# Kernel tuning notes

Hardware: AMD Instinct MI355X
Metric: run time of the kernel (lower is better)

The kernel has to match this reference:

```python
import jax, jax.numpy as jnp
import numpy as np

B, N, D, H = 2, 512, 384, 12
SQK, SV, PQ, PV = 16, 16, 4, 8
SCALE = 1.0 / np.sqrt(SQK + 4 * PQ)  # attention_scale, point_pair_dim=4
EPS = 1e-12


def setup_inputs() -> dict:
    key = jax.random.key(0)
    ks = jax.random.split(key, 10)

    def w(k, fan_in, fan_out):
        return (jax.random.normal(k, (fan_in, fan_out), jnp.float32) / np.sqrt(fan_in))

    return {
        "hidden": jax.random.normal(ks[0], (B, N, D), jnp.float32),
        "xyz": jax.random.normal(ks[1], (B, N, 3), jnp.float32),
        "W_qk": w(ks[2], D, 2 * H * SQK), "b_qk": jnp.zeros((2 * H * SQK,), jnp.float32),
        "W_vs": w(ks[3], D, H * SV), "b_vs": jnp.zeros((H * SV,), jnp.float32),
        "W_so": w(ks[4], H * SV, D), "b_so": jnp.zeros((D,), jnp.float32),
        "W_pqk": w(ks[5], D, H * PQ * 3), "b_pqk": jnp.zeros((H * PQ * 3,), jnp.float32),
        "W_pv": w(ks[6], D, H * PV * 3), "b_pv": jnp.zeros((H * PV * 3,), jnp.float32),
        "W_po": w(ks[7], H * PV * 3, D), "b_po": jnp.zeros((D,), jnp.float32),
        "W_fp": w(ks[8], 2 * D, D), "b_fp": jnp.zeros((D,), jnp.float32),
    }


def reference(hidden, xyz, W_qk, b_qk, W_vs, b_vs, W_so, b_so,
              W_pqk, b_pqk, W_pv, b_pv, W_po, b_po, W_fp, b_fp):
    # scalar q/k/v (note: heads are NOT split in the attention matmuls, per source)
    qk = hidden @ W_qk + b_qk                       # [B,N,2*H*SQK]
    q_s, k_s = jnp.split(qk, 2, axis=-1)            # [B,N,H*SQK] each
    v_s = hidden @ W_vs + b_vs                      # [B,N,H*SV]

    # points; k_points = q_points in source
    qp = (hidden @ W_pqk + b_pqk).reshape(B, N, H, PQ, 3)
    vp = hidden @ W_pv + b_pv                       # [B,N,H*PV*3]

    scalar_attn = jnp.einsum('bid,bjd->bij', q_s, k_s)  # [B,N,N]

    # fused pairwise point features: dist(q_i, k_j) + sum of 3 cosine components
    # = dist + cos_sim, per (head, point); avoid materializing [B,N,N,H,P,3].
    dot = jnp.einsum('bihpc,bjhpc->bijhp', qp, qp)      # [B,N,N,H,PQ]
    n2 = jnp.sum(qp * qp, axis=-1)                      # [B,N,H,PQ]
    d2 = n2[:, :, None] + n2[:, None] - 2.0 * dot
    dist = jnp.sqrt(jnp.maximum(d2, 0.0) + EPS)
    nrm = jnp.sqrt(n2 + EPS)
    cos = dot / (nrm[:, :, None] * nrm[:, None])
    point_attn = jnp.sum(dist + cos, axis=(-1, -2))     # [B,N,N]

    attn = jax.nn.softmax((scalar_attn + point_attn) * SCALE, axis=-1)

    scalar_result = jnp.einsum('bij,bjd->bid', attn, v_s)   # [B,N,H*SV]
    point_result = jnp.einsum('bij,bjd->bid', attn, vp)     # [B,N,H*PV*3]

    scalar_result = scalar_result @ W_so + b_so             # [B,N,D]
    point_result = point_result @ W_po + b_po               # [B,N,D]

    result = jnp.concatenate([scalar_result, point_result], axis=-1) @ W_fp + b_fp
    delta_xyz = point_result.reshape(B, N, -1, 3).mean(axis=2)  # [B,N,3]
    return result, xyz + delta_xyz
```

## Files before the change

kernel.cpp:

```cpp
#include <hip/hip_runtime.h>
#include <math.h>

typedef unsigned short u16;
typedef __attribute__((ext_vector_type(8))) short bf16x8;
typedef __attribute__((ext_vector_type(4))) float f32x4;

#define BB 2
#define NN 512
#define SCALEF 0.17677669529663687f

__device__ __forceinline__ u16 f2bf(float x) {
  union { float f; unsigned u; } c; c.f = x;
  unsigned r = (c.u + 0x7FFFu + ((c.u >> 16) & 1u)) >> 16;
  return (u16)r;
}
__device__ __forceinline__ float bf2f(u16 h) {
  union { unsigned u; float f; } c; c.u = ((unsigned)h) << 16;
  return c.f;
}
__device__ __forceinline__ void pack8(const float* v, bf16x8& h, bf16x8& l) {
#pragma unroll
  for (int j = 0; j < 8; ++j) {
    u16 hi = f2bf(v[j]);
    h[j] = (short)hi;
    l[j] = (short)f2bf(v[j] - bf2f(hi));
  }
}
#define MFMA3(ACC, AH, AL, BH, BL)                                              \
  ACC = __builtin_amdgcn_mfma_f32_16x16x32_bf16(AH, BH, ACC, 0, 0, 0);          \
  ACC = __builtin_amdgcn_mfma_f32_16x16x32_bf16(AH, BL, ACC, 0, 0, 0);          \
  ACC = __builtin_amdgcn_mfma_f32_16x16x32_bf16(AL, BH, ACC, 0, 0, 0);

template<int MR, int NF>
__device__ __forceinline__ void mfma_tile(
    const u16* __restrict__ Ah, const u16* __restrict__ Al, int lda,
    const u16* __restrict__ Bh, const u16* __restrict__ Bl, int ldb,
    int kBeg, int kEnd, int arow, int bcol, f32x4 (&acc)[MR][NF]) {
  const int lane = threadIdx.x & 63;
  const int rr = lane & 15, kg = lane >> 4;
  const u16* pah = Ah + (size_t)(arow + rr) * lda + kg * 8;
  const u16* pal = Al + (size_t)(arow + rr) * lda + kg * 8;
  const u16* pbh = Bh + (size_t)(bcol + rr) * ldb + kg * 8;
  const u16* pbl = Bl + (size_t)(bcol + rr) * ldb + kg * 8;
#pragma unroll 2
  for (int k0 = kBeg; k0 < kEnd; k0 += 32) {
    bf16x8 a_h[MR], a_l[MR], b_h[NF], b_l[NF];
#pragma unroll
    for (int m = 0; m < MR; ++m) {
      a_h[m] = *(const bf16x8*)(pah + (size_t)m * 16 * lda + k0);
      a_l[m] = *(const bf16x8*)(pal + (size_t)m * 16 * lda + k0);
    }
#pragma unroll
    for (int f = 0; f < NF; ++f) {
      b_h[f] = *(const bf16x8*)(pbh + (size_t)f * 16 * ldb + k0);
      b_l[f] = *(const bf16x8*)(pbl + (size_t)f * 16 * ldb + k0);
    }
#pragma unroll
    for (int m = 0; m < MR; ++m)
#pragma unroll
      for (int f = 0; f < NF; ++f) { MFMA3(acc[m][f], a_h[m], a_l[m], b_h[f], b_l[f]) }
  }
}

__global__ __launch_bounds__(512) void k_input(
    const float* __restrict__ hidden, const float* __restrict__ xyz,
    const float* __restrict__ W_qk, const float* __restrict__ b_qk,
    const float* __restrict__ W_vs, const float* __restrict__ b_vs,
    const float* __restrict__ W_pv, const float* __restrict__ b_pv,
    const float* __restrict__ W_pqk, const float* __restrict__ b_pqk,
    u16* __restrict__ QKh, u16* __restrict__ QKl,
    u16* __restrict__ VTh, u16* __restrict__ VTl,
    float* __restrict__ QPf, float* __restrict__ out_xyz) {
  __shared__ f32x4 CB[7][2][3][64];
  __shared__ u16 Dh[48][32], Dl[48][32];
  const int tid = threadIdx.x;
  const int w = tid >> 6, lane = tid & 63;
  const int rr = lane & 15, kg = lane >> 4;
  const int row0 = blockIdx.y * 32, col0 = blockIdx.x * 48;

  if (blockIdx.x == 18) {
    for (int t2 = tid; t2 < 96; t2 += 512)
      out_xyz[(size_t)row0 * 3 + t2] = xyz[(size_t)row0 * 3 + t2];
  }

  const float* W; const float* bias; int Ns, region;
  if (col0 < 384)      { W = W_qk;  Ns = 384; bias = b_qk + col0;          W += col0;       region = 0; }
  else if (col0 < 576) { W = W_vs;  Ns = 192; bias = b_vs + (col0 - 384);  W += col0 - 384; region = 1; }
  else if (col0 < 864) { W = W_pv;  Ns = 288; bias = b_pv + (col0 - 576);  W += col0 - 576; region = 1; }
  else                 { W = W_pqk; Ns = 144; bias = b_pqk + (col0 - 864); W += col0 - 864; region = 2; }

  f32x4 acc[2][3] = {};
  const float* pa = hidden + (size_t)(row0 + rr) * 384 + kg * 8;
  const float* pw = W + rr;
  for (int k0 = w * 32; k0 < 384; k0 += 256) {
    bf16x8 a_h[2], a_l[2], b_h[3], b_l[3];
#pragma unroll
    for (int m = 0; m < 2; ++m) {
      float v[8];
      *(float4*)&v[0] = *(const float4*)(pa + (size_t)m * 16 * 384 + k0);
      *(float4*)&v[4] = *(const float4*)(pa + (size_t)m * 16 * 384 + k0 + 4);
      pack8(v, a_h[m], a_l[m]);
    }
    const float* bp0 = pw + (size_t)(k0 + kg * 8) * Ns;
#pragma unroll
    for (int f = 0; f < 3; ++f) {
      float v[8];
#pragma unroll
      for (int j = 0; j < 8; ++j) v[j] = bp0[(size_t)j * Ns + f * 16];
      pack8(v, b_h[f], b_l[f]);
    }
#pragma unroll
    for (int m = 0; m < 2; ++m)
#pragma unroll
      for (int f = 0; f < 3; ++f) { MFMA3(acc[m][f], a_h[m], a_l[m], b_h[f], b_l[f]) }
  }
  if (w) {
#pragma unroll
    for (int m = 0; m < 2; ++m)
#pragma unroll
      for (int f = 0; f < 3; ++f) CB[w - 1][m][f][lane] = acc[m][f];
  }
  __syncthreads();
  if (w) return;
#pragma unroll
  for (int wv = 0; wv < 7; ++wv)
#pragma unroll
    for (int m = 0; m < 2; ++m)
#pragma unroll
      for (int f = 0; f < 3; ++f) acc[m][f] += CB[wv][m][f][lane];

  const int rb = (lane >> 4) << 2, cc = lane & 15;
  if (region == 0) {
#pragma unroll
    for (int f = 0; f < 3; ++f) {
      int n = col0 + f * 16 + cc;
      float bv = bias[f * 16 + cc];
#pragma unroll
      for (int m = 0; m < 2; ++m)
#pragma unroll
        for (int r = 0; r < 4; ++r) {
          float v = acc[m][f][r] + bv;
          int row = row0 + m * 16 + rb + r;
          u16 hi = f2bf(v);
          QKh[(size_t)row * 384 + n] = hi;
          QKl[(size_t)row * 384 + n] = f2bf(v - bf2f(hi));
        }
    }
  } else if (region == 2) {
#pragma unroll
    for (int f = 0; f < 3; ++f) {
      int c = (col0 - 864) + f * 16 + cc;
      float bv = bias[f * 16 + cc];
#pragma unroll
      for (int m = 0; m < 2; ++m)
#pragma unroll
        for (int r = 0; r < 4; ++r)
          QPf[(size_t)(row0 + m * 16 + rb + r) * 144 + c] = acc[m][f][r] + bv;
    }
  } else {
#pragma unroll
    for (int f = 0; f < 3; ++f) {
      float bv = bias[f * 16 + cc];
#pragma unroll
      for (int m = 0; m < 2; ++m)
#pragma unroll
        for (int r = 0; r < 4; ++r) {
          float v = acc[m][f][r] + bv;
          u16 hi = f2bf(v);
          Dh[f * 16 + cc][m * 16 + rb + r] = hi;
          Dl[f * 16 + cc][m * 16 + rb + r] = f2bf(v - bf2f(hi));
        }
    }
    const int b = row0 >> 9, rl = row0 & 511;
    const int cbase = col0 - 384;
    u16* dsth = VTh + (size_t)b * 480 * 512;
    u16* dstl = VTl + (size_t)b * 480 * 512;
    for (int u = lane; u < 192; u += 64) {
      int c = u >> 2, seg = u & 3;
      *(uint4*)(dsth + (size_t)(cbase + c) * 512 + rl + seg * 8) = *(const uint4*)&Dh[c][seg * 8];
      *(uint4*)(dstl + (size_t)(cbase + c) * 512 + rl + seg * 8) = *(const uint4*)&Dl[c][seg * 8];
    }
  }
}

#define PROW 244
__global__ __launch_bounds__(512) void k_attn(
    const u16* __restrict__ QKh, const u16* __restrict__ QKl,
    const float* __restrict__ QPf, float* __restrict__ ATTf) {
  __shared__ float Pi[32][PROW];
  __shared__ float Pj[32][PROW];
  __shared__ float Sf[2][32 * 33];
  const int b = blockIdx.z;
  int t = blockIdx.x, ti_ = 0;
  while (t >= 16 - ti_) { t -= 16 - ti_; ++ti_; }
  const int tj_ = ti_ + t;
  const int i0 = ti_ * 32, j0 = tj_ * 32;
  const bool offdiag = (tj_ != ti_);
  const int tid = threadIdx.x;
  for (int u = tid; u < 3072; u += 512) {
    int side = (u >= 1536) ? 1 : 0;
    int rem = u - side * 1536;
    int row = rem / 48, hp = rem - row * 48;
    int grow = b * NN + (side ? j0 : i0) + row;
    const float* p = QPf + (size_t)grow * 144 + hp * 3;
    float x = p[0], y = p[1], z = p[2];
    float n2 = x * x + y * y + z * z;
    float inv = __frsqrt_rn(n2 + 1e-12f);
    float* dst = side ? &Pj[row][0] : &Pi[row][0];
    ((float4*)dst)[hp] = make_float4(x, y, z, n2);
    dst[192 + hp] = inv;
  }
  __syncthreads();
  const int h = tid >> 8;
  const int t8 = tid & 255;
  const int tj = t8 & 15, ti = t8 >> 4;
  {
    float a00 = 0.f, a01 = 0.f, a10 = 0.f, a11 = 0.f;
    const float4* A0 = (const float4*)&Pi[ti][0];
    const float4* A1 = (const float4*)&Pi[ti + 16][0];
    const float4* B0 = (const float4*)&Pj[tj][0];
    const float4* B1 = (const float4*)&Pj[tj + 16][0];
    const float* iA0 = &Pi[ti][192];
    const float* iA1 = &Pi[ti + 16][192];
    const float* iB0 = &Pj[tj][192];
    const float* iB1 = &Pj[tj + 16][192];
    const int hpB = h * 24, hpE = hpB + 24;
#pragma unroll 4
    for (int hp = hpB; hp < hpE; ++hp) {
      float4 p0 = A0[hp], p1 = A1[hp], q0 = B0[hp], q1 = B1[hp];
      float va0 = iA0[hp], va1 = iA1[hp], vb0 = iB0[hp], vb1 = iB1[hp];
      {
        float dot = p0.x * q0.x + p0.y * q0.y + p0.z * q0.z;
        float d2 = fmaxf(fmaf(-2.f, dot, p0.w + q0.w), 0.f) + 1e-12f;
        a00 += d2 * __frsqrt_rn(d2) + dot * (va0 * vb0);
      }
      {
        float dot = p0.x * q1.x + p0.y * q1.y + p0.z * q1.z;
        float d2 = fmaxf(fmaf(-2.f, dot, p0.w + q1.w), 0.f) + 1e-12f;
        a01 += d2 * __frsqrt_rn(d2) + dot * (va0 * vb1);
      }
      {
        float dot = p1.x * q0.x + p1.y * q0.y + p1.z * q0.z;
        float d2 = fmaxf(fmaf(-2.f, dot, p1.w + q0.w), 0.f) + 1e-12f;
        a10 += d2 * __frsqrt_rn(d2) + dot * (va1 * vb0);
      }
      {
        float dot = p1.x * q1.x + p1.y * q1.y + p1.z * q1.z;
        float d2 = fmaxf(fmaf(-2.f, dot, p1.w + q1.w), 0.f) + 1e-12f;
        a11 += d2 * __frsqrt_rn(d2) + dot * (va1 * vb1);
      }
    }
    Sf[h][ti * 33 + tj] = a00;
    Sf[h][ti * 33 + tj + 16] = a01;
    Sf[h][(ti + 16) * 33 + tj] = a10;
    Sf[h][(ti + 16) * 33 + tj + 16] = a11;
  }
  const int w = tid >> 6, lane = tid & 63;
  const int dir = w >> 2, sub = w & 3;
  f32x4 q[1][1] = {};
  if (dir == 0) {
    int arow = b * NN + i0 + (sub >> 1) * 16;
    int brow = b * NN + j0 + (sub & 1) * 16;
    mfma_tile<1, 1>(QKh, QKl, 384, QKh + 192, QKl + 192, 384, 0, 192, arow, brow, q);
  } else if (offdiag) {
    int arow = b * NN + j0 + (sub >> 1) * 16;
    int brow = b * NN + i0 + (sub & 1) * 16;
    mfma_tile<1, 1>(QKh, QKl, 384, QKh + 192, QKl + 192, 384, 0, 192, arow, brow, q);
  }
  __syncthreads();
  const int rl = (sub >> 1) * 16 + ((lane >> 4) << 2);
  const int cl = (sub & 1) * 16 + (lane & 15);
  float* Cb = ATTf + (size_t)b * NN * NN;
  if (dir == 0) {
#pragma unroll
    for (int r = 0; r < 4; ++r)
      Cb[(size_t)(i0 + rl + r) * NN + j0 + cl] =
          q[0][0][r] + Sf[0][(rl + r) * 33 + cl] + Sf[1][(rl + r) * 33 + cl];
  } else if (offdiag) {
#pragma unroll
    for (int r = 0; r < 4; ++r)
      Cb[(size_t)(j0 + rl + r) * NN + i0 + cl] =
          q[0][0][r] + Sf[0][cl * 33 + rl + r] + Sf[1][cl * 33 + rl + r];
  }
}

__global__ __launch_bounds__(512) void k_pv(
    const float* __restrict__ ATTf,
    const u16* __restrict__ VTh, const u16* __restrict__ VTl,
    u16* __restrict__ SRh, u16* __restrict__ SRl) {
  __shared__ f32x4 CB[7][3][64];
  __shared__ float RS[7][64];
  const int tid = threadIdx.x;
  const int w = tid >> 6, lane = tid & 63;
  const int rr = lane & 15, kg = lane >> 4;
  const int b = blockIdx.z;
  const int row0 = blockIdx.y * 16, col0 = blockIdx.x * 48;
  const float* pa = ATTf + (size_t)(b * NN + row0 + rr) * NN + kg * 8;
  const u16* pbh = VTh + (size_t)b * 480 * 512 + (size_t)(col0 + rr) * 512 + kg * 8;
  const u16* pbl = VTl + (size_t)b * 480 * 512 + (size_t)(col0 + rr) * 512 + kg * 8;
  f32x4 acc[3] = {};
  float rs = 0.f;
  for (int k0 = w * 32; k0 < NN; k0 += 256) {
    bf16x8 a_h, a_l, b_h[3], b_l[3];
    {
      float v[8];
      *(float4*)&v[0] = *(const float4*)(pa + k0);
      *(float4*)&v[4] = *(const float4*)(pa + k0 + 4);
#pragma unroll
      for (int j = 0; j < 8; ++j) { float e = __expf(v[j] * SCALEF); rs += e; v[j] = e; }
      pack8(v, a_h, a_l);
    }
#pragma unroll
    for (int f = 0; f < 3; ++f) {
      b_h[f] = *(const bf16x8*)(pbh + (size_t)f * 16 * 512 + k0);
      b_l[f] = *(const bf16x8*)(pbl + (size_t)f * 16 * 512 + k0);
    }
#pragma unroll
    for (int f = 0; f < 3; ++f) { MFMA3(acc[f], a_h, a_l, b_h[f], b_l[f]) }
  }
  if (w) {
#pragma unroll
    for (int f = 0; f < 3; ++f) CB[w - 1][f][lane] = acc[f];
    RS[w - 1][lane] = rs;
  }
  __syncthreads();
  if (w) return;
#pragma unroll
  for (int wv = 0; wv < 7; ++wv) {
#pragma unroll
    for (int f = 0; f < 3; ++f) acc[f] += CB[wv][f][lane];
    rs += RS[wv][lane];
  }
  rs += __shfl_xor(rs, 16);
  rs += __shfl_xor(rs, 32);
  const int rb = (lane >> 4) << 2, cc = lane & 15;
  float inv[4];
#pragma unroll
  for (int r = 0; r < 4; ++r) inv[r] = 1.0f / __shfl(rs, rb + r);
  u16* oh = SRh + (size_t)b * NN * 480;
  u16* ol = SRl + (size_t)b * NN * 480;
#pragma unroll
  for (int f = 0; f < 3; ++f) {
    int n = col0 + f * 16 + cc;
#pragma unroll
    for (int r = 0; r < 4; ++r) {
      float v = acc[f][r] * inv[r];
      u16 hi = f2bf(v);
      oh[(size_t)(row0 + rb + r) * 480 + n] = hi;
      ol[(size_t)(row0 + rb + r) * 480 + n] = f2bf(v - bf2f(hi));
    }
  }
}

__global__ __launch_bounds__(512) void k_outproj(
    const u16* __restrict__ SRh, const u16* __restrict__ SRl,
    const float* __restrict__ W_so, const float* __restrict__ b_so,
    const float* __restrict__ W_po, const float* __restrict__ b_po,
    u16* __restrict__ PRh, u16* __restrict__ PRl, float* __restrict__ out_xyz) {
  __shared__ f32x4 CB[7][3][64];
  __shared__ float D[16][49];
  const int tid = threadIdx.x;
  const int w = tid >> 6, lane = tid & 63;
  const int rr = lane & 15, kg = lane >> 4;
  const int t = blockIdx.x;
  const int row0 = blockIdx.y * 16, col0 = t * 48;
  const float* W = (t < 8) ? W_so : W_po;
  const int kBeg = (t < 8) ? 0 : 192, kEnd = (t < 8) ? 192 : 480;
  const int wcol = (t < 8) ? col0 : col0 - 384;
  const u16* pah = SRh + (size_t)(row0 + rr) * 480 + kg * 8;
  const u16* pal = SRl + (size_t)(row0 + rr) * 480 + kg * 8;
  const float* pw = W + wcol + rr;
  f32x4 acc[3] = {};
  for (int k0 = kBeg + w * 32; k0 < kEnd; k0 += 256) {
    bf16x8 a_h, a_l, b_h[3], b_l[3];
    a_h = *(const bf16x8*)(pah + k0);
    a_l = *(const bf16x8*)(pal + k0);
    const float* bp0 = pw + (size_t)(k0 - kBeg + kg * 8) * 384;
#pragma unroll
    for (int f = 0; f < 3; ++f) {
      float v[8];
#pragma unroll
      for (int j = 0; j < 8; ++j) v[j] = bp0[(size_t)j * 384 + f * 16];
      pack8(v, b_h[f], b_l[f]);
    }
#pragma unroll
    for (int f = 0; f < 3; ++f) { MFMA3(acc[f], a_h, a_l, b_h[f], b_l[f]) }
  }
  if (w) {
#pragma unroll
    for (int f = 0; f < 3; ++f) CB[w - 1][f][lane] = acc[f];
  }
  __syncthreads();
  if (w) return;
#pragma unroll
  for (int wv = 0; wv < 7; ++wv)
#pragma unroll
    for (int f = 0; f < 3; ++f) acc[f] += CB[wv][f][lane];
  const int rb = (lane >> 4) << 2, cc = lane & 15;
#pragma unroll
  for (int f = 0; f < 3; ++f) {
    int n = col0 + f * 16 + cc;
    float bias = (n < 384) ? b_so[n] : b_po[n - 384];
#pragma unroll
    for (int r = 0; r < 4; ++r) {
      float v = acc[f][r] + bias;
      u16 hi = f2bf(v);
      PRh[(size_t)(row0 + rb + r) * 768 + n] = hi;
      PRl[(size_t)(row0 + rb + r) * 768 + n] = f2bf(v - bf2f(hi));
      if (t >= 8) D[rb + r][f * 16 + cc] = v;
    }
  }
  if (t >= 8 && lane < 16) {
    float sx = 0.f, sy = 0.f, sz = 0.f;
#pragma unroll
    for (int p = 0; p < 16; ++p) {
      sx += D[lane][3 * p];
      sy += D[lane][3 * p + 1];
      sz += D[lane][3 * p + 2];
    }
    int token = row0 + lane;
    atomicAdd(out_xyz + (size_t)token * 3 + 0, sx * (1.0f / 128.f));
    atomicAdd(out_xyz + (size_t)token * 3 + 1, sy * (1.0f / 128.f));
    atomicAdd(out_xyz + (size_t)token * 3 + 2, sz * (1.0f / 128.f));
  }
}

__global__ __launch_bounds__(512) void k_final(
    const u16* __restrict__ PRh, const u16* __restrict__ PRl,
    const float* __restrict__ W_fp, const float* __restrict__ b_fp,
    float* __restrict__ out_res) {
  __shared__ f32x4 CB[7][3][64];
  const int tid = threadIdx.x;
  const int w = tid >> 6, lane = tid & 63;
  const int rr = lane & 15, kg = lane >> 4;
  const int row0 = blockIdx.y * 16, col0 = blockIdx.x * 48;
  const u16* pah = PRh + (size_t)(row0 + rr) * 768 + kg * 8;
  const u16* pal = PRl + (size_t)(row0 + rr) * 768 + kg * 8;
  const float* pw = W_fp + col0 + rr;
  f32x4 acc[3] = {};
  for (int k0 = w * 32; k0 < 768; k0 += 256) {
    bf16x8 a_h, a_l, b_h[3], b_l[3];
    a_h = *(const bf16x8*)(pah + k0);
    a_l = *(const bf16x8*)(pal + k0);
    const float* bp0 = pw + (size_t)(k0 + kg * 8) * 384;
#pragma unroll
    for (int f = 0; f < 3; ++f) {
      float v[8];
#pragma unroll
      for (int j = 0; j < 8; ++j) v[j] = bp0[(size_t)j * 384 + f * 16];
      pack8(v, b_h[f], b_l[f]);
    }
#pragma unroll
    for (int f = 0; f < 3; ++f) { MFMA3(acc[f], a_h, a_l, b_h[f], b_l[f]) }
  }
  if (w) {
#pragma unroll
    for (int f = 0; f < 3; ++f) CB[w - 1][f][lane] = acc[f];
  }
  __syncthreads();
  if (w) return;
#pragma unroll
  for (int wv = 0; wv < 7; ++wv)
#pragma unroll
    for (int f = 0; f < 3; ++f) acc[f] += CB[wv][f][lane];
  const int rb = (lane >> 4) << 2, cc = lane & 15;
#pragma unroll
  for (int f = 0; f < 3; ++f) {
    int n = col0 + f * 16 + cc;
#pragma unroll
    for (int r = 0; r < 4; ++r)
      out_res[(size_t)(row0 + rb + r) * 384 + n] = acc[f][r] + b_fp[n];
  }
}

extern "C" void kernel_launch(void* const* d_in, const int* in_sizes, int n_in,
                              void* d_out, int out_size, void* d_ws, size_t ws_size,
                              hipStream_t stream) {
  const float* hidden = (const float*)d_in[0];
  const float* xyz   = (const float*)d_in[1];
  const float* W_qk  = (const float*)d_in[2];
  const float* b_qk  = (const float*)d_in[3];
  const float* W_vs  = (const float*)d_in[4];
  const float* b_vs  = (const float*)d_in[5];
  const float* W_so  = (const float*)d_in[6];
  const float* b_so  = (const float*)d_in[7];
  const float* W_pqk = (const float*)d_in[8];
  const float* b_pqk = (const float*)d_in[9];
  const float* W_pv  = (const float*)d_in[10];
  const float* b_pv  = (const float*)d_in[11];
  const float* W_po  = (const float*)d_in[12];
  const float* b_po  = (const float*)d_in[13];
  const float* W_fp  = (const float*)d_in[14];
  const float* b_fp  = (const float*)d_in[15];

  float* out_res = (float*)d_out;
  float* out_xyz = out_res + (size_t)BB * NN * 384;

  u16* p   = (u16*)d_ws;
  u16* QKh = p;            p += 393216;
  u16* QKl = p;            p += 393216;
  u16* VTh = p;            p += 491520;
  u16* VTl = p;            p += 491520;
  u16* SRh = p;            p += 491520;
  u16* SRl = p;            p += 491520;
  u16* PRh = p;            p += 786432;
  u16* PRl = p;            p += 786432;
  float* QPf  = (float*)p; p += 2 * 147456;
  float* ATTf = (float*)p;

  k_input<<<dim3(21, 32), 512, 0, stream>>>(hidden, xyz,
                                            W_qk, b_qk, W_vs, b_vs, W_pv, b_pv, W_pqk, b_pqk,
                                            QKh, QKl, VTh, VTl, QPf, out_xyz);
  k_attn<<<dim3(136, 1, 2), 512, 0, stream>>>(QKh, QKl, QPf, ATTf);
  k_pv<<<dim3(10, 32, 2), 512, 0, stream>>>(ATTf, VTh, VTl, SRh, SRl);
  k_outproj<<<dim3(16, 64), 512, 0, stream>>>(SRh, SRl, W_so, b_so, W_po, b_po,
                                              PRh, PRl, out_xyz);
  k_final<<<dim3(8, 64), 512, 0, stream>>>(PRh, PRl, W_fp, b_fp, out_res);
}
```

Before: 71.03 us.

## Fold output projections into final projection via precomputed combined weight matrix

The scalar and point output projections are composed with the final projection into a single 480x384 weight matrix, plus a combined bias and a reduced xyz-delta weight. Extra blocks in the input-projection kernel compute these each call. This removes one GEMM launch and the intermediate PR round trip through memory, so the tail becomes one GEMM with a small side path for xyz. The cost is extra weight-product work inside the first kernel, a bias loop that runs serially over 768 terms, and a change in rounding because the fused weights are split into bf16 hi/lo.

```diff
diff --git a/kernel.cpp b/kernel.cpp
--- a/kernel.cpp
+++ b/kernel.cpp
@@ -63,25 +63,99 @@
 }
 
 __global__ __launch_bounds__(512) void k_input(
-    const float* __restrict__ hidden, const float* __restrict__ xyz,
+    const float* __restrict__ hidden,
     const float* __restrict__ W_qk, const float* __restrict__ b_qk,
     const float* __restrict__ W_vs, const float* __restrict__ b_vs,
     const float* __restrict__ W_pv, const float* __restrict__ b_pv,
     const float* __restrict__ W_pqk, const float* __restrict__ b_pqk,
+    const float* __restrict__ W_so, const float* __restrict__ b_so,
+    const float* __restrict__ W_po, const float* __restrict__ b_po,
+    const float* __restrict__ W_fp, const float* __restrict__ b_fp,
     u16* __restrict__ QKh, u16* __restrict__ QKl,
     u16* __restrict__ VTh, u16* __restrict__ VTl,
-    float* __restrict__ QPf, float* __restrict__ out_xyz) {
+    float* __restrict__ QPf,
+    u16* __restrict__ WCTh, u16* __restrict__ WCTl,
+    float* __restrict__ bc, float* __restrict__ Wdf) {
+  const int tid = threadIdx.x;
+  if (blockIdx.x >= 21) {
+    const int cx = blockIdx.x - 21, ky = blockIdx.y;
+    if (cx < 8 && ky < 10) {
+      const int w = tid >> 6, lane = tid & 63;
+      if (w >= 3) return;
+      const int rr = lane & 15, kg = lane >> 4;
+      const int c0 = cx * 48;
+      const int kbase = ky * 48 + w * 16;
+      const float* Wop; int moff;
+      if (kbase < 192) { Wop = W_so + (size_t)kbase * 384; moff = 0; }
+      else             { Wop = W_po + (size_t)(kbase - 192) * 384; moff = 384; }
+      f32x4 acc[3] = {};
+      const float* pa = Wop + (size_t)rr * 384 + kg * 8;
+      const float* pw = W_fp + (size_t)moff * 384 + c0 + rr;
+      for (int m0 = 0; m0 < 384; m0 += 32) {
+        bf16x8 a_h, a_l, b_h[3], b_l[3];
+        float v[8];
+        *(float4*)&v[0] = *(const float4*)(pa + m0);
+        *(float4*)&v[4] = *(const float4*)(pa + m0 + 4);
+        pack8(v, a_h, a_l);
+        const float* bp0 = pw + (size_t)(m0 + kg * 8) * 384;
+#pragma unroll
+        for (int f = 0; f < 3; ++f) {
+          float u[8];
+#pragma unroll
+          for (int j = 0; j < 8; ++j) u[j] = bp0[(size_t)j * 384 + f * 16];
+          pack8(u, b_h[f], b_l[f]);
+        }
+#pragma unroll
+        for (int f = 0; f < 3; ++f) { MFMA3(acc[f], a_h, a_l, b_h[f], b_l[f]) }
+      }
+      const int rb = (lane >> 4) << 2, cc = lane & 15;
+#pragma unroll
+      for (int f = 0; f < 3; ++f) {
+        int c = c0 + f * 16 + cc;
+#pragma unroll
+        for (int r = 0; r < 4; ++r) {
+          int k = kbase + rb + r;
+          float vv = acc[f][r];
+          u16 hi = f2bf(vv);
+          WCTh[(size_t)c * 480 + k] = hi;
+          WCTl[(size_t)c * 480 + k] = f2bf(vv - bf2f(hi));
+        }
+      }
+      return;
+    }
+    if (cx == 0 && ky == 10) {
+      if (tid < 384) {
+        float s = b_fp[tid];
+        for (int m = 0; m < 384; ++m) s += b_so[m] * W_fp[(size_t)m * 384 + tid];
+        for (int m = 0; m < 384; ++m) s += b_po[m] * W_fp[(size_t)(384 + m) * 384 + tid];
+        bc[tid] = s;
+      }
+      return;
+    }
+    if (cx == 1 && ky == 10) {
+      for (int idx = tid; idx < 867; idx += 512) {
+        if (idx < 864) {
+          int j = idx / 3, c = idx - j * 3;
+          float s = 0.f;
+          for (int k = 0; k < 128; ++k) s += W_po[(size_t)j * 384 + 3 * k + c];
+          Wdf[idx] = s * (1.0f / 128.f);
+        } else {
+          int c = idx - 864;
+          float s = 0.f;
+          for (int k = 0; k < 128; ++k) s += b_po[3 * k + c];
+          Wdf[idx] = s * (1.0f / 128.f);
+        }
+      }
+      return;
+    }
+    return;
+  }
+
   __shared__ f32x4 CB[7][2][3][64];
   __shared__ u16 Dh[48][32], Dl[48][32];
-  const int tid = threadIdx.x;
   const int w = tid >> 6, lane = tid & 63;
   const int rr = lane & 15, kg = lane >> 4;
   const int row0 = blockIdx.y * 32, col0 = blockIdx.x * 48;
-
-  if (blockIdx.x == 18) {
-    for (int t2 = tid; t2 < 96; t2 += 512)
-      out_xyz[(size_t)row0 * 3 + t2] = xyz[(size_t)row0 * 3 + t2];
-  }
 
   const float* W; const float* bias; int Ns, region;
   if (col0 < 384)      { W = W_qk;  Ns = 384; bias = b_qk + col0;          W += col0;       region = 0; }
@@ -352,36 +426,51 @@
   }
 }
 
-__global__ __launch_bounds__(512) void k_outproj(
+__global__ __launch_bounds__(512) void k_tail(
     const u16* __restrict__ SRh, const u16* __restrict__ SRl,
-    const float* __restrict__ W_so, const float* __restrict__ b_so,
-    const float* __restrict__ W_po, const float* __restrict__ b_po,
-    u16* __restrict__ PRh, u16* __restrict__ PRl, float* __restrict__ out_xyz) {
+    const u16* __restrict__ WCTh, const u16* __restrict__ WCTl,
+    const float* __restrict__ bc, const float* __restrict__ Wdf,
+    const float* __restrict__ xyz,
+    float* __restrict__ out_res, float* __restrict__ out_xyz) {
+  const int tid = threadIdx.x;
+  const int row0 = blockIdx.y * 16;
+  if (blockIdx.x == 8) {
+    if (tid < 384) {
+      int out = tid >> 3, part = tid & 7;
+      int lt = out / 3, c = out - lt * 3;
+      int token = row0 + lt;
+      const u16* sh = SRh + (size_t)token * 480 + 192 + part * 36;
+      const u16* sl = SRl + (size_t)token * 480 + 192 + part * 36;
+      float s = 0.f;
+#pragma unroll 4
+      for (int kk = 0; kk < 36; ++kk) {
+        float v = bf2f(sh[kk]) + bf2f(sl[kk]);
+        s += v * Wdf[(part * 36 + kk) * 3 + c];
+      }
+#pragma unroll
+      for (int d = 4; d; d >>= 1) s += __shfl_down(s, d, 8);
+      if (part == 0)
+        out_xyz[(size_t)token * 3 + c] = xyz[(size_t)token * 3 + c] + s + Wdf[864 + c];
+    }
+    return;
+  }
   __shared__ f32x4 CB[7][3][64];
-  __shared__ float D[16][49];
-  const int tid = threadIdx.x;
   const int w = tid >> 6, lane = tid & 63;
   const int rr = lane & 15, kg = lane >> 4;
-  const int t = blockIdx.x;
-  const int row0 = blockIdx.y * 16, col0 = t * 48;
-  const float* W = (t < 8) ? W_so : W_po;
-  const int kBeg = (t < 8) ? 0 : 192, kEnd = (t < 8) ? 192 : 480;
-  const int wcol = (t < 8) ? col0 : col0 - 384;
+  const int col0 = blockIdx.x * 48;
   const u16* pah = SRh + (size_t)(row0 + rr) * 480 + kg * 8;
   const u16* pal = SRl + (size_t)(row0 + rr) * 480 + kg * 8;
-  const float* pw = W + wcol + rr;
+  const u16* pbh = WCTh + (size_t)(col0 + rr) * 480 + kg * 8;
+  const u16* pbl = WCTl + (size_t)(col0 + rr) * 480 + kg * 8;
   f32x4 acc[3] = {};
-  for (int k0 = kBeg + w * 32; k0 < kEnd; k0 += 256) {
+  for (int k0 = w * 32; k0 < 480; k0 += 256) {
     bf16x8 a_h, a_l, b_h[3], b_l[3];
     a_h = *(const bf16x8*)(pah + k0);
     a_l = *(const bf16x8*)(pal + k0);
-    const float* bp0 = pw + (size_t)(k0 - kBeg + kg * 8) * 384;
 #pragma unroll
     for (int f = 0; f < 3; ++f) {
-      float v[8];
-#pragma unroll
-      for (int j = 0; j < 8; ++j) v[j] = bp0[(size_t)j * 384 + f * 16];
-      pack8(v, b_h[f], b_l[f]);
+      b_h[f] = *(const bf16x8*)(pbh + (size_t)f * 16 * 480 + k0);
+      b_l[f] = *(const bf16x8*)(pbl + (size_t)f * 16 * 480 + k0);
     }
 #pragma unroll
     for (int f = 0; f < 3; ++f) { MFMA3(acc[f], a_h, a_l, b_h[f], b_l[f]) }
@@ -400,76 +489,9 @@
 #pragma unroll
   for (int f = 0; f < 3; ++f) {
     int n = col0 + f * 16 + cc;
-    float bias = (n < 384) ? b_so[n] : b_po[n - 384];
-#pragma unroll
-    for (int r = 0; r < 4; ++r) {
-      float v = acc[f][r] + bias;
-      u16 hi = f2bf(v);
-      PRh[(size_t)(row0 + rb + r) * 768 + n] = hi;
-      PRl[(size_t)(row0 + rb + r) * 768 + n] = f2bf(v - bf2f(hi));
-      if (t >= 8) D[rb + r][f * 16 + cc] = v;
-    }
-  }
-  if (t >= 8 && lane < 16) {
-    float sx = 0.f, sy = 0.f, sz = 0.f;
-#pragma unroll
-    for (int p = 0; p < 16; ++p) {
-      sx += D[lane][3 * p];
-      sy += D[lane][3 * p + 1];
-      sz += D[lane][3 * p + 2];
-    }
-    int token = row0 + lane;
-    atomicAdd(out_xyz + (size_t)token * 3 + 0, sx * (1.0f / 128.f));
-    atomicAdd(out_xyz + (size_t)token * 3 + 1, sy * (1.0f / 128.f));
-    atomicAdd(out_xyz + (size_t)token * 3 + 2, sz * (1.0f / 128.f));
-  }
-}
-
-__global__ __launch_bounds__(512) void k_final(
-    const u16* __restrict__ PRh, const u16* __restrict__ PRl,
-    const float* __restrict__ W_fp, const float* __restrict__ b_fp,
-    float* __restrict__ out_res) {
-  __shared__ f32x4 CB[7][3][64];
-  const int tid = threadIdx.x;
-  const int w = tid >> 6, lane = tid & 63;
-  const int rr = lane & 15, kg = lane >> 4;
-  const int row0 = blockIdx.y * 16, col0 = blockIdx.x * 48;
-  const u16* pah = PRh + (size_t)(row0 + rr) * 768 + kg * 8;
-  const u16* pal = PRl + (size_t)(row0 + rr) * 768 + kg * 8;
-  const float* pw = W_fp + col0 + rr;
-  f32x4 acc[3] = {};
-  for (int k0 = w * 32; k0 < 768; k0 += 256) {
-    bf16x8 a_h, a_l, b_h[3], b_l[3];
-    a_h = *(const bf16x8*)(pah + k0);
-    a_l = *(const bf16x8*)(pal + k0);
-    const float* bp0 = pw + (size_t)(k0 + kg * 8) * 384;
-#pragma unroll
-    for (int f = 0; f < 3; ++f) {
-      float v[8];
-#pragma unroll
-      for (int j = 0; j < 8; ++j) v[j] = bp0[(size_t)j * 384 + f * 16];
-      pack8(v, b_h[f], b_l[f]);
-    }
-#pragma unroll
-    for (int f = 0; f < 3; ++f) { MFMA3(acc[f], a_h, a_l, b_h[f], b_l[f]) }
-  }
-  if (w) {
-#pragma unroll
-    for (int f = 0; f < 3; ++f) CB[w - 1][f][lane] = acc[f];
-  }
-  __syncthreads();
-  if (w) return;
-#pragma unroll
-  for (int wv = 0; wv < 7; ++wv)
-#pragma unroll
-    for (int f = 0; f < 3; ++f) acc[f] += CB[wv][f][lane];
-  const int rb = (lane >> 4) << 2, cc = lane & 15;
-#pragma unroll
-  for (int f = 0; f < 3; ++f) {
-    int n = col0 + f * 16 + cc;
 #pragma unroll
     for (int r = 0; r < 4; ++r)
-      out_res[(size_t)(row0 + rb + r) * 384 + n] = acc[f][r] + b_fp[n];
+      out_res[(size_t)(row0 + rb + r) * 384 + n] = acc[f][r] + bc[n];
   }
 }
 
@@ -497,23 +519,25 @@
   float* out_xyz = out_res + (size_t)BB * NN * 384;
 
   u16* p   = (u16*)d_ws;
-  u16* QKh = p;            p += 393216;
-  u16* QKl = p;            p += 393216;
-  u16* VTh = p;            p += 491520;
-  u16* VTl = p;            p += 491520;
-  u16* SRh = p;            p += 491520;
-  u16* SRl = p;            p += 491520;
-  u16* PRh = p;            p += 786432;
-  u16* PRl = p;            p += 786432;
+  u16* QKh  = p;           p += 393216;
+  u16* QKl  = p;           p += 393216;
+  u16* VTh  = p;           p += 491520;
+  u16* VTl  = p;           p += 491520;
+  u16* SRh  = p;           p += 491520;
+  u16* SRl  = p;           p += 491520;
+  u16* WCTh = p;           p += 184320;
+  u16* WCTl = p;           p += 184320;
   float* QPf  = (float*)p; p += 2 * 147456;
-  float* ATTf = (float*)p;
-
-  k_input<<<dim3(21, 32), 512, 0, stream>>>(hidden, xyz,
+  float* ATTf = (float*)p; p += 2 * 524288;
+  float* bcf  = (float*)p; p += 2 * 384;
+  float* Wdf  = (float*)p;
+
+  k_input<<<dim3(29, 32), 512, 0, stream>>>(hidden,
                                             W_qk, b_qk, W_vs, b_vs, W_pv, b_pv, W_pqk, b_pqk,
-                                            QKh, QKl, VTh, VTl, QPf, out_xyz);
+                                            W_so, b_so, W_po, b_po, W_fp, b_fp,
+                                            QKh, QKl, VTh, VTl, QPf, WCTh, WCTl, bcf, Wdf);
   k_attn<<<dim3(136, 1, 2), 512, 0, stream>>>(QKh, QKl, QPf, ATTf);
   k_pv<<<dim3(10, 32, 2), 512, 0, stream>>>(ATTf, VTh, VTl, SRh, SRl);
-  k_outproj<<<dim3(16, 64), 512, 0, stream>>>(SRh, SRl, W_so, b_so, W_po, b_po,
-                                              PRh, PRl, out_xyz);
-  k_final<<<dim3(8, 64), 512, 0, stream>>>(PRh, PRl, W_fp, b_fp, out_res);
-}
+  k_tail<<<dim3(9, 64), 512, 0, stream>>>(SRh, SRl, WCTh, WCTl, bcf, Wdf, xyz,
+                                          out_res, out_xyz);
+}
```

Measured after the change: 86.33 us. 1.22x slower.
